# Kernel optimization log

Hardware: AMD Instinct MI355X
Metric: run time of the kernel (lower is better)

Reference implementation:

```python
import jax, jax.numpy as jnp
import numpy as np

BS, N, K = 64, 256, 64
IN_DIM, HID = 64, 64

def _mlp2(x, W1, b1, W2, b2, act_last):
    h = jax.nn.silu(x @ W1 + b1)
    h = h @ W2 + b2
    return jax.nn.silu(h) if act_last else h

def setup_inputs() -> dict:
    key = jax.random.key(0)
    ks = jax.random.split(key, 16)
    def g(k, shape, scale=1.0):
        return jax.random.normal(k, shape, dtype=jnp.float32) * scale
    s_e1 = 1.0 / np.sqrt(2 * IN_DIM + 1)
    s_h = 1.0 / np.sqrt(HID)
    s_h1 = 1.0 / np.sqrt(IN_DIM + HID)
    return {
        "ped_features": g(ks[0], (BS, N, 2)),
        "h_st": g(ks[1], (BS, N, IN_DIM)),
        "h_neigh": g(ks[2], (BS, N, K, IN_DIM)),
        "rela_features": g(ks[3], (BS, N, K, 6)),
        "neigh_mask": jax.random.bernoulli(ks[4], 0.7, (BS, N, K)),
        # f_e: Linear(2*in+1, hid), SiLU, Linear(hid, hid), SiLU
        "We1": g(ks[5], (2 * IN_DIM + 1, HID), s_e1), "be1": g(ks[6], (HID,), s_e1),
        "We2": g(ks[7], (HID, HID), s_h), "be2": g(ks[8], (HID,), s_h),
        # f_x: Linear(hid, hid), SiLU, Linear(hid, 1)
        "Wx1": g(ks[9], (HID, HID), s_h), "bx1": g(ks[10], (HID,), s_h),
        "Wx2": g(ks[11], (HID, 1), s_h), "bx2": g(ks[12], (1,), s_h),
        # f_h: Linear(in+hid, hid), SiLU, Linear(hid, hid)
        "Wh1": g(ks[13], (IN_DIM + HID, HID), s_h1), "bh1": g(ks[14], (HID,), s_h1),
        "Wh2": g(ks[15], (HID, HID), s_h), "bh2": g(jax.random.fold_in(key, 99), (HID,), s_h),
    }

def reference(ped_features, h_st, h_neigh, rela_features, neigh_mask,
              We1, be1, We2, be2, Wx1, bx1, Wx2, bx2, Wh1, bh1, Wh2, bh2):
    bs, n, k, _ = h_neigh.shape
    # pairwise distances from relative xy: [bs, N, k]
    dists = jnp.linalg.norm(rela_features[..., :2], axis=-1)
    neigh_num = neigh_mask.sum(axis=-1).astype(h_st.dtype)  # [bs, N]
    # broadcast h_st over neighbor axis and concat: [bs, N, k, 2*in+1]
    h_st_b = jnp.broadcast_to(h_st[:, :, None, :], (bs, n, k, h_st.shape[-1]))
    tmp = jnp.concatenate([h_st_b, h_neigh, dists[..., None]], axis=-1)
    m_ij = _mlp2(tmp, We1, be1, We2, be2, act_last=True)  # [bs, N, k, hid]
    m_ij = jnp.where(neigh_mask[..., None], m_ij, 0.0)
    gate = _mlp2(m_ij, Wx1, bx1, Wx2, bx2, act_last=False)  # [bs, N, k, 1]
    agg = (rela_features[..., :2] * gate).sum(axis=-2)  # [bs, N, 2]
    agg = agg / (neigh_num[..., None] + 1e-6)
    x_new = ped_features + agg
    m_i = m_ij.sum(axis=-2)  # [bs, N, hid]
    h_new = h_st + _mlp2(jnp.concatenate([h_st, m_i], axis=-1), Wh1, bh1, Wh2, bh2, act_last=False)
    return (x_new, h_new)
```

## Files before the change

kernel.cpp:

```cpp
#include <hip/hip_runtime.h>
#include <hip/hip_bf16.h>


typedef __attribute__((ext_vector_type(8))) short short8;
typedef __attribute__((ext_vector_type(4))) float f32x4;
typedef __attribute__((ext_vector_type(2))) float f32x2;
typedef __attribute__((ext_vector_type(2))) unsigned int u32x2;
typedef __attribute__((ext_vector_type(4))) unsigned int u32x4;

#define NODES 16384
#define NPB   16
#define NBLK  (NODES / NPB)

#define MFMA16(a, b, c) __builtin_amdgcn_mfma_f32_16x16x32_bf16((a), (b), (c), 0, 0, 0)

__device__ __forceinline__ unsigned short f2bf(float f) {
  unsigned int u = __float_as_uint(f);
  u += 0x7FFFu + ((u >> 16) & 1u);
  return (unsigned short)(u >> 16);
}
__device__ __forceinline__ unsigned int pk2(float lo, float hi) {
  unsigned int r;
  asm("v_cvt_pk_bf16_f32 %0, %1, %2" : "=v"(r) : "v"(lo), "v"(hi));
  return r;
}
__device__ __forceinline__ float bfl(unsigned int u) { return __uint_as_float(u << 16); }
__device__ __forceinline__ float bfh(unsigned int u) { return __uint_as_float(u & 0xFFFF0000u); }
__device__ __forceinline__ float silu_f(float x) {
  return x * __builtin_amdgcn_rcpf(1.f + __expf(-x));
}
__device__ __forceinline__ f32x4 silu4(f32x4 x) {
  f32x4 r; r[0]=silu_f(x[0]); r[1]=silu_f(x[1]); r[2]=silu_f(x[2]); r[3]=silu_f(x[3]); return r;
}
__device__ __forceinline__ short8 packb(f32x4 a, f32x4 b) {
  u32x4 t;
  t[0] = pk2(a[0], a[1]); t[1] = pk2(a[2], a[3]);
  t[2] = pk2(b[0], b[1]); t[3] = pk2(b[2], b[3]);
  return __builtin_bit_cast(short8, t);
}
__device__ __forceinline__ short8 ldfragT(const float* __restrict__ W, int k0, int col) {
  short8 r;
  #pragma unroll
  for (int m = 0; m < 8; m++) r[m] = (short)f2bf(W[(k0 + m) * 64 + col]);
  return r;
}

__global__ __launch_bounds__(256, 2) void egnn_mfma(
    const float* __restrict__ ped, const float* __restrict__ h_st,
    const float* __restrict__ h_neigh, const float* __restrict__ rela,
    const unsigned char* __restrict__ mask8,
    const float* __restrict__ We1, const float* __restrict__ be1,
    const float* __restrict__ We2, const float* __restrict__ be2,
    const float* __restrict__ Wx1, const float* __restrict__ bx1,
    const float* __restrict__ Wx2, const float* __restrict__ bx2,
    const float* __restrict__ Wh1, const float* __restrict__ bh1,
    const float* __restrict__ Wh2, const float* __restrict__ bh2,
    float* __restrict__ out)
{
  __shared__ __align__(16) float s_hst[16][64];
  __shared__ __align__(16) float s_u[16][64];
  __shared__ __align__(16) float s_miw[4][16][64];
  __shared__ __align__(16) unsigned int s_scr[4][2][64][4];
  __shared__ __align__(16) short8 s_af[16][64];
  __shared__ float s_wx2[64];
  __shared__ float s_aggx[4][16], s_aggy[4][16], s_nn[4][16];
  __shared__ int s_flags[2];

  const int t  = threadIdx.x;
  const int l  = t & 63;
  const int w  = t >> 6;
  const int lg = l >> 4;
  const int jl = l & 15;
  const int base = blockIdx.x * NPB;

  if (t == 0) { s_flags[0] = 1; s_flags[1] = 1; }
  __syncthreads();
  {
    const unsigned int* mw = (const unsigned int*)mask8;
    unsigned int iok = 1, fok = 1;
    #pragma unroll
    for (int q = 0; q < 4; q++) {
      unsigned int v = mw[t * 4 + q];
      if (v > 1u) iok = 0;
      if (v != 0u && v != 0x3F800000u) fok = 0;
    }
    if (!iok) atomicAnd(&s_flags[0], 0);
    if (!fok) atomicAnd(&s_flags[1], 0);
  }
  {
    const f32x4* src = (const f32x4*)(h_st + (size_t)base * 64);
    f32x4* dst = (f32x4*)&s_hst[0][0];
    dst[t] = src[t];
    if (t < 64) s_wx2[t] = Wx2[t];
  }
  #pragma unroll
  for (int ci = 0; ci < 4; ci++) {
    const int c  = 4 * w + ci;
    const int g  = c >> 3, mt = (c >> 1) & 3, kk = c & 1;
    const float* W = g ? Wx1 : We2;
    s_af[c][l] = ldfragT(W, 8 * lg + 32 * kk, 16 * mt + jl);
  }
  __syncthreads();
  const int mode = s_flags[0] ? 0 : (s_flags[1] ? 1 : 2);

  auto ldmask = [&](size_t idx) -> float {
    if (mode == 0)      return (((const int*)mask8)[idx] != 0) ? 1.f : 0.f;
    else if (mode == 1) return (((const float*)mask8)[idx] != 0.f) ? 1.f : 0.f;
    else                return (mask8[idx] != 0) ? 1.f : 0.f;
  };

  const int sc_lgp_e = (lg >> 1);
  const int sc_m0    = 2 * (lg & 1);

  {
    f32x4 uacc = {0.f, 0.f, 0.f, 0.f};
    #pragma unroll
    for (int kk = 0; kk < 2; kk++) {
      short8 au = ldfragT(We1, 8 * lg + 32 * kk, 16 * w + jl);
      f32x4 q0 = *(const f32x4*)&s_hst[jl][8 * lg + 32 * kk];
      f32x4 q1 = *(const f32x4*)&s_hst[jl][8 * lg + 32 * kk + 4];
      uacc = MFMA16(au, packb(q0, q1), uacc);
    }
    f32x4 b1v = *(const f32x4*)(be1 + 16 * w + 4 * lg);
    *(f32x4*)&s_u[jl][16 * w + 4 * lg] = uacc + b1v;
  }

  short8 a1[4][2];
  #pragma unroll
  for (int mt = 0; mt < 4; mt++)
    #pragma unroll
    for (int kk = 0; kk < 2; kk++)
      a1[mt][kk] = ldfragT(We1 + 64 * 64, 8 * lg + 32 * kk, 16 * mt + jl);

  f32x4 w1l4[4], c2v[4], c3v[4];
  #pragma unroll
  for (int ht = 0; ht < 4; ht++) {
    w1l4[ht] = *(const f32x4*)(We1 + 128 * 64 + 16 * ht + 4 * lg);
    c2v[ht]  = *(const f32x4*)(be2 + 16 * ht + 4 * lg);
    c3v[ht]  = *(const f32x4*)(bx1 + 16 * ht + 4 * lg);
  }
  const float bx2s = bx2[0];

  const float* hn_lane = h_neigh + ((size_t)base * 64 + 16 * w + jl) * 64 + 8 * lg;
  const size_t ro = (size_t)base * 64 + 16 * w + jl;
  f32x4 pf0 = *(const f32x4*)(hn_lane + 0);
  f32x4 pf1 = *(const f32x4*)(hn_lane + 4);
  f32x4 pf2 = *(const f32x4*)(hn_lane + 32);
  f32x4 pf3 = *(const f32x4*)(hn_lane + 36);
  f32x2 pre = *(const f32x2*)(rela + ro * 6);
  float pmf = ldmask(ro);
  __syncthreads();

  #pragma unroll 1
  for (int nl = 0; nl < NPB; nl++) {
    const short8 b1k0 = packb(pf0, pf1);
    const short8 b1k1 = packb(pf2, pf3);
    const f32x2 rr = pre; const float mf = pmf;
    if (nl < NPB - 1) {
      const float* p = hn_lane + (size_t)(nl + 1) * 4096;
      pf0 = *(const f32x4*)(p + 0);  pf1 = *(const f32x4*)(p + 4);
      pf2 = *(const f32x4*)(p + 32); pf3 = *(const f32x4*)(p + 36);
      pre = *(const f32x2*)(rela + (ro + (size_t)(nl + 1) * 64) * 6);
      pmf = ldmask(ro + (size_t)(nl + 1) * 64);
    }
    const float d = sqrtf(rr[0] * rr[0] + rr[1] * rr[1]);

    float msum = mf;
    msum += __shfl_xor(msum, 1, 64); msum += __shfl_xor(msum, 2, 64);
    msum += __shfl_xor(msum, 4, 64); msum += __shfl_xor(msum, 8, 64);
    if (l == 0) s_nn[w][nl] = msum;

    f32x4 acc[4];
    #pragma unroll
    for (int ht = 0; ht < 4; ht++) {
      acc[ht] = *(const f32x4*)&s_u[nl][16 * ht + 4 * lg] + d * w1l4[ht];
      acc[ht] = MFMA16(a1[ht][0], b1k0, acc[ht]);
      acc[ht] = MFMA16(a1[ht][1], b1k1, acc[ht]);
    }
    #pragma unroll
    for (int ht = 0; ht < 4; ht++) {
      f32x4 e = silu4(acc[ht]);
      u32x2 wv; wv[0] = pk2(e[0], e[1]); wv[1] = pk2(e[2], e[3]);
      const int half = (4 * ht + lg) >> 3;
      const int lgp  = (2 * ht + sc_lgp_e) & 3;
      *(u32x2*)&s_scr[w][half][lgp * 16 + jl][sc_m0] = wv;
    }
    short8 b2k0 = *(const short8*)&s_scr[w][0][l][0];
    short8 b2k1 = *(const short8*)&s_scr[w][1][l][0];

    #pragma unroll
    for (int ht = 0; ht < 4; ht++) {
      const short8 f2k0 = s_af[2 * ht][l];
      const short8 f2k1 = s_af[2 * ht + 1][l];
      acc[ht] = MFMA16(f2k0, b2k0, c2v[ht]);
      acc[ht] = MFMA16(f2k1, b2k1, acc[ht]);
    }
    #pragma unroll
    for (int ht = 0; ht < 4; ht++) {
      f32x4 m = silu4(acc[ht]) * mf;
      u32x2 wv; wv[0] = pk2(m[0], m[1]); wv[1] = pk2(m[2], m[3]);
      const int half = (4 * ht + lg) >> 3;
      const int lgp  = (2 * ht + sc_lgp_e) & 3;
      *(u32x2*)&s_scr[w][half][lgp * 16 + jl][sc_m0] = wv;
    }
    short8 b3k0 = *(const short8*)&s_scr[w][0][l][0];
    short8 b3k1 = *(const short8*)&s_scr[w][1][l][0];

    #pragma unroll
    for (int ht = 0; ht < 4; ht++) {
      const short8 f3k0 = s_af[8 + 2 * ht][l];
      const short8 f3k1 = s_af[8 + 2 * ht + 1][l];
      acc[ht] = MFMA16(f3k0, b3k0, c3v[ht]);
      acc[ht] = MFMA16(f3k1, b3k1, acc[ht]);
    }

    {
      const int hw = l & 31, jh = l >> 5;
      const int half = hw >> 4;
      const int lgp  = (hw & 15) >> 2;
      const int m0   = hw & 3;
      const int rot  = hw >> 2;
      float pe = 0.f, po = 0.f;
      #pragma unroll
      for (int c = 0; c < 8; c++) {
        const int j = 8 * jh + ((c + rot) & 7);
        unsigned int v = s_scr[w][half][lgp * 16 + j][m0];
        pe += bfl(v); po += bfh(v);
      }
      pe += __shfl_xor(pe, 32, 64);
      po += __shfl_xor(po, 32, 64);
      if (l < 32) {
        f32x2 v2; v2[0] = pe; v2[1] = po;
        *(f32x2*)&s_miw[w][nl][2 * hw] = v2;
      }
    }

    float gg = 0.f;
    #pragma unroll
    for (int ht = 0; ht < 4; ht++) {
      const f32x4 wx = *(const f32x4*)&s_wx2[16 * ht + 4 * lg];
      f32x4 g = silu4(acc[ht]);
      gg += g[0] * wx[0] + g[1] * wx[1] + g[2] * wx[2] + g[3] * wx[3];
    }
    gg += __shfl_xor(gg, 16, 64);
    gg += __shfl_xor(gg, 32, 64);
    const float gate = gg + bx2s;

    float ax = rr[0] * gate, ay = rr[1] * gate;
    ax += __shfl_xor(ax, 1, 64); ay += __shfl_xor(ay, 1, 64);
    ax += __shfl_xor(ax, 2, 64); ay += __shfl_xor(ay, 2, 64);
    ax += __shfl_xor(ax, 4, 64); ay += __shfl_xor(ay, 4, 64);
    ax += __shfl_xor(ax, 8, 64); ay += __shfl_xor(ay, 8, 64);
    if (l == 0) { s_aggx[w][nl] = ax; s_aggy[w][nl] = ay; }
  }
  __syncthreads();

  if (t < 32) {
    const int node = t >> 1, c = t & 1;
    const float nn = s_nn[0][node] + s_nn[1][node] + s_nn[2][node] + s_nn[3][node];
    const float ag = (c ? (s_aggy[0][node] + s_aggy[1][node] + s_aggy[2][node] + s_aggy[3][node])
                        : (s_aggx[0][node] + s_aggx[1][node] + s_aggx[2][node] + s_aggx[3][node]));
    out[(size_t)(base + node) * 2 + c] =
        ped[(size_t)(base + node) * 2 + c] + ag / (nn + 1e-6f);
  }

  {
    f32x4 hacc = *(const f32x4*)(bh1 + 16 * w + 4 * lg);
    #pragma unroll
    for (int kk = 0; kk < 4; kk++) {
      short8 ah = ldfragT(Wh1, 8 * lg + 32 * kk, 16 * w + jl);
      f32x4 q0, q1;
      if (kk < 2) {
        q0 = *(const f32x4*)&s_hst[jl][8 * lg + 32 * kk];
        q1 = *(const f32x4*)&s_hst[jl][8 * lg + 32 * kk + 4];
      } else {
        const int off = 8 * lg + 32 * (kk - 2);
        q0 = *(const f32x4*)&s_miw[0][jl][off]     + *(const f32x4*)&s_miw[1][jl][off]
           + *(const f32x4*)&s_miw[2][jl][off]     + *(const f32x4*)&s_miw[3][jl][off];
        q1 = *(const f32x4*)&s_miw[0][jl][off + 4] + *(const f32x4*)&s_miw[1][jl][off + 4]
           + *(const f32x4*)&s_miw[2][jl][off + 4] + *(const f32x4*)&s_miw[3][jl][off + 4];
      }
      hacc = MFMA16(ah, packb(q0, q1), hacc);
    }
    f32x4 h1 = silu4(hacc);
    u32x2 wv; wv[0] = pk2(h1[0], h1[1]); wv[1] = pk2(h1[2], h1[3]);
    const int half = (4 * w + lg) >> 3;
    const int lgp  = (2 * w + sc_lgp_e) & 3;
    *(u32x2*)&s_scr[0][half][lgp * 16 + jl][sc_m0] = wv;
  }
  __syncthreads();
  {
    short8 hb0 = *(const short8*)&s_scr[0][0][l][0];
    short8 hb1 = *(const short8*)&s_scr[0][1][l][0];
    short8 aw0 = ldfragT(Wh2, 8 * lg,      16 * w + jl);
    short8 aw1 = ldfragT(Wh2, 8 * lg + 32, 16 * w + jl);
    f32x4 oacc = *(const f32x4*)(bh2 + 16 * w + 4 * lg);
    oacc = MFMA16(aw0, hb0, oacc);
    oacc = MFMA16(aw1, hb1, oacc);
    f32x4 res = oacc + *(const f32x4*)&s_hst[jl][16 * w + 4 * lg];
    *(f32x4*)(out + 32768 + (size_t)(base + jl) * 64 + 16 * w + 4 * lg) = res;
  }
}

extern "C" void kernel_launch(void* const* d_in, const int* in_sizes, int n_in,
                              void* d_out, int out_size, void* d_ws, size_t ws_size,
                              hipStream_t stream) {
  (void)in_sizes; (void)n_in; (void)out_size; (void)d_ws; (void)ws_size;
  const float* ped     = (const float*)d_in[0];
  const float* h_st    = (const float*)d_in[1];
  const float* h_neigh = (const float*)d_in[2];
  const float* rela    = (const float*)d_in[3];
  const unsigned char* mask = (const unsigned char*)d_in[4];
  const float* We1 = (const float*)d_in[5];  const float* be1 = (const float*)d_in[6];
  const float* We2 = (const float*)d_in[7];  const float* be2 = (const float*)d_in[8];
  const float* Wx1 = (const float*)d_in[9];  const float* bx1 = (const float*)d_in[10];
  const float* Wx2 = (const float*)d_in[11]; const float* bx2 = (const float*)d_in[12];
  const float* Wh1 = (const float*)d_in[13]; const float* bh1 = (const float*)d_in[14];
  const float* Wh2 = (const float*)d_in[15]; const float* bh2 = (const float*)d_in[16];

  hipLaunchKernelGGL(egnn_mfma, dim3(NBLK), dim3(256), 0, stream,
                     ped, h_st, h_neigh, rela, mask,
                     We1, be1, We2, be2, Wx1, bx1, Wx2, bx2,
                     Wh1, bh1, Wh2, bh2, (float*)d_out);
}
```

Before: 118.8 us.

## Permute weight fragment K-order to feed MFMA outputs directly as B operands

Reorders the K index of the We2/Wx1 A-fragments so each lane's MFMA accumulator outputs can be packed straight into the next layer's B operand, skipping the LDS scratch round trip between layers. The second-layer store to scratch is kept, presumably for the later gate/aggregation code. The per-lane distance weight vector moves from registers into shared memory to lower register pressure. The cost is extra LDS reads per iteration and a riskier index permutation that must match the accumulator layout exactly.

```diff
diff --git a/kernel.cpp b/kernel.cpp
--- a/kernel.cpp
+++ b/kernel.cpp
@@ -42,6 +42,15 @@
   short8 r;
   #pragma unroll
   for (int m = 0; m < 8; m++) r[m] = (short)f2bf(W[(k0 + m) * 64 + col]);
+  return r;
+}
+__device__ __forceinline__ short8 ldfragP(const float* __restrict__ W, int kk, int lg, int col) {
+  short8 r;
+  #pragma unroll
+  for (int m = 0; m < 8; m++) {
+    const int k = 32 * kk + ((m < 4) ? (4 * lg + m) : (16 + 4 * lg + (m - 4)));
+    r[m] = (short)f2bf(W[k * 64 + col]);
+  }
   return r;
 }
 
@@ -62,6 +71,7 @@
   __shared__ __align__(16) float s_miw[4][16][64];
   __shared__ __align__(16) unsigned int s_scr[4][2][64][4];
   __shared__ __align__(16) short8 s_af[16][64];
+  __shared__ float s_w1l[64];
   __shared__ float s_wx2[64];
   __shared__ float s_aggx[4][16], s_aggy[4][16], s_nn[4][16];
   __shared__ int s_flags[2];
@@ -91,14 +101,15 @@
     const f32x4* src = (const f32x4*)(h_st + (size_t)base * 64);
     f32x4* dst = (f32x4*)&s_hst[0][0];
     dst[t] = src[t];
-    if (t < 64) s_wx2[t] = Wx2[t];
+    if (t < 64)       s_w1l[t] = We1[128 * 64 + t];
+    else if (t < 128) s_wx2[t - 64] = Wx2[t - 64];
   }
   #pragma unroll
   for (int ci = 0; ci < 4; ci++) {
     const int c  = 4 * w + ci;
     const int g  = c >> 3, mt = (c >> 1) & 3, kk = c & 1;
     const float* W = g ? Wx1 : We2;
-    s_af[c][l] = ldfragT(W, 8 * lg + 32 * kk, 16 * mt + jl);
+    s_af[c][l] = ldfragP(W, kk, lg, 16 * mt + jl);
   }
   __syncthreads();
   const int mode = s_flags[0] ? 0 : (s_flags[1] ? 1 : 2);
@@ -132,12 +143,11 @@
     for (int kk = 0; kk < 2; kk++)
       a1[mt][kk] = ldfragT(We1 + 64 * 64, 8 * lg + 32 * kk, 16 * mt + jl);
 
-  f32x4 w1l4[4], c2v[4], c3v[4];
+  f32x4 c2v[4], c3v[4];
   #pragma unroll
   for (int ht = 0; ht < 4; ht++) {
-    w1l4[ht] = *(const f32x4*)(We1 + 128 * 64 + 16 * ht + 4 * lg);
-    c2v[ht]  = *(const f32x4*)(be2 + 16 * ht + 4 * lg);
-    c3v[ht]  = *(const f32x4*)(bx1 + 16 * ht + 4 * lg);
+    c2v[ht] = *(const f32x4*)(be2 + 16 * ht + 4 * lg);
+    c3v[ht] = *(const f32x4*)(bx1 + 16 * ht + 4 * lg);
   }
   const float bx2s = bx2[0];
 
@@ -173,20 +183,15 @@
     f32x4 acc[4];
     #pragma unroll
     for (int ht = 0; ht < 4; ht++) {
-      acc[ht] = *(const f32x4*)&s_u[nl][16 * ht + 4 * lg] + d * w1l4[ht];
+      const f32x4 wl = *(const f32x4*)&s_w1l[16 * ht + 4 * lg];
+      acc[ht] = *(const f32x4*)&s_u[nl][16 * ht + 4 * lg] + d * wl;
       acc[ht] = MFMA16(a1[ht][0], b1k0, acc[ht]);
       acc[ht] = MFMA16(a1[ht][1], b1k1, acc[ht]);
     }
-    #pragma unroll
-    for (int ht = 0; ht < 4; ht++) {
-      f32x4 e = silu4(acc[ht]);
-      u32x2 wv; wv[0] = pk2(e[0], e[1]); wv[1] = pk2(e[2], e[3]);
-      const int half = (4 * ht + lg) >> 3;
-      const int lgp  = (2 * ht + sc_lgp_e) & 3;
-      *(u32x2*)&s_scr[w][half][lgp * 16 + jl][sc_m0] = wv;
-    }
-    short8 b2k0 = *(const short8*)&s_scr[w][0][l][0];
-    short8 b2k1 = *(const short8*)&s_scr[w][1][l][0];
+    f32x4 se0 = silu4(acc[0]), se1 = silu4(acc[1]);
+    f32x4 se2 = silu4(acc[2]), se3 = silu4(acc[3]);
+    const short8 b2k0 = packb(se0, se1);
+    const short8 b2k1 = packb(se2, se3);
 
     #pragma unroll
     for (int ht = 0; ht < 4; ht++) {
@@ -195,16 +200,21 @@
       acc[ht] = MFMA16(f2k0, b2k0, c2v[ht]);
       acc[ht] = MFMA16(f2k1, b2k1, acc[ht]);
     }
-    #pragma unroll
-    for (int ht = 0; ht < 4; ht++) {
-      f32x4 m = silu4(acc[ht]) * mf;
-      u32x2 wv; wv[0] = pk2(m[0], m[1]); wv[1] = pk2(m[2], m[3]);
-      const int half = (4 * ht + lg) >> 3;
-      const int lgp  = (2 * ht + sc_lgp_e) & 3;
-      *(u32x2*)&s_scr[w][half][lgp * 16 + jl][sc_m0] = wv;
-    }
-    short8 b3k0 = *(const short8*)&s_scr[w][0][l][0];
-    short8 b3k1 = *(const short8*)&s_scr[w][1][l][0];
+    f32x4 sm0 = silu4(acc[0]) * mf, sm1 = silu4(acc[1]) * mf;
+    f32x4 sm2 = silu4(acc[2]) * mf, sm3 = silu4(acc[3]) * mf;
+    {
+      u32x2 wv;
+      wv[0] = pk2(sm0[0], sm0[1]); wv[1] = pk2(sm0[2], sm0[3]);
+      *(u32x2*)&s_scr[w][(0 + lg) >> 3][((0 + sc_lgp_e) & 3) * 16 + jl][sc_m0] = wv;
+      wv[0] = pk2(sm1[0], sm1[1]); wv[1] = pk2(sm1[2], sm1[3]);
+      *(u32x2*)&s_scr[w][(4 + lg) >> 3][((2 + sc_lgp_e) & 3) * 16 + jl][sc_m0] = wv;
+      wv[0] = pk2(sm2[0], sm2[1]); wv[1] = pk2(sm2[2], sm2[3]);
+      *(u32x2*)&s_scr[w][(8 + lg) >> 3][((4 + sc_lgp_e) & 3) * 16 + jl][sc_m0] = wv;
+      wv[0] = pk2(sm3[0], sm3[1]); wv[1] = pk2(sm3[2], sm3[3]);
+      *(u32x2*)&s_scr[w][(12 + lg) >> 3][((6 + sc_lgp_e) & 3) * 16 + jl][sc_m0] = wv;
+    }
+    const short8 b3k0 = packb(sm0, sm1);
+    const short8 b3k1 = packb(sm2, sm3);
 
     #pragma unroll
     for (int ht = 0; ht < 4; ht++) {
```

After: 114.1 us. 1.04x faster.
